# Optimization experiments

Hardware: AMD Instinct MI355X
Metric: run time of the kernel (lower is better)

## Reference

```python
import jax, jax.numpy as jnp
import numpy as np

B, L, D = 8, 4096, 1024   # batch, max words, sent_dim
S, SENT_LEN = 255, 16     # sentences per sample, words per sentence (255*16=4080)
START_BOUND = 1           # leading zero-pad region, as in the torch module


def setup_inputs() -> dict:
    key = jax.random.key(0)
    k1, k2, k3, k4 = jax.random.split(key, 4)
    words_emb = jax.random.normal(k1, (B, L, D), jnp.float32)
    sents_emb = jax.random.normal(k2, (B, S, D), jnp.float32)
    # nn.Linear(2D, D): weight [D, 2D], bias [D]
    W1_w = jax.random.normal(k3, (D, 2 * D), jnp.float32) / np.sqrt(2 * D)
    W1_b = jax.random.normal(k4, (D,), jnp.float32) * 0.01
    # sentence-index-per-word map; -1 marks the zero-padded regions
    sm = -np.ones((B, L), np.int32)
    idx = np.repeat(np.arange(S, dtype=np.int32), SENT_LEN)  # [S*SENT_LEN]
    sm[:, START_BOUND:START_BOUND + S * SENT_LEN] = idx
    sent_map = jnp.asarray(sm)
    return {"words_emb": words_emb, "sents_emb": sents_emb,
            "W1_w": W1_w, "W1_b": W1_b, "sent_map": sent_map}


def reference(words_emb, sents_emb, W1_w, W1_b, sent_map):
    # Expand sentence embeddings to word positions via gather; zero outside spans.
    valid = sent_map >= 0                                    # [B, L]
    safe_idx = jnp.clip(sent_map, 0)                         # [B, L]
    gathered = jnp.take_along_axis(sents_emb, safe_idx[..., None], axis=1)  # [B, L, D]
    sents_state_flat = jnp.where(valid[..., None], gathered, 0.0)
    # concat word + sentence features, then Linear + ReLU
    x = jnp.concatenate([words_emb, sents_state_flat], axis=-1)  # [B, L, 2D]
    return jax.nn.relu(jnp.einsum('ble,de->bld', x, W1_w) + W1_b)
```

## Files before the change

### kernel.cpp

```cpp
#include <hip/hip_runtime.h>
#include <stdint.h>

constexpr int kB = 8;
constexpr int kL = 4096;
constexpr int kD = 1024;
constexpr int kS = 255;
constexpr int kM = kB * kL;
constexpr int kK = 2 * kD;
constexpr int kN = kD;

typedef __bf16 bf16x8 __attribute__((ext_vector_type(8)));
typedef float  f32x4  __attribute__((ext_vector_type(4)));

constexpr size_t WS_WORDS = 0;
constexpr size_t WS_SENTS = WS_WORDS + (size_t)kM * kD * 2;
constexpr size_t WS_W     = WS_SENTS + (size_t)kB * kS * kD * 2;
constexpr size_t WS_ZP    = WS_W + (size_t)kN * kK * 2;
constexpr size_t WS_NEED  = WS_ZP + 3072;

__device__ __forceinline__ uint32_t pk_bf16x2(float a, float b) {
    uint32_t ua = __float_as_uint(a) + 0x8000u;
    uint32_t ub = __float_as_uint(b) + 0x8000u;
    return __builtin_amdgcn_perm(ub, ua, 0x07060302u);
}

__device__ __forceinline__ void async16(const void* g, void* l) {
    __builtin_amdgcn_global_load_lds(
        (const __attribute__((address_space(1))) uint32_t*)g,
        (__attribute__((address_space(3))) uint32_t*)l, 16, 0, 0);
}

#define WAITVM(n)  asm volatile("s_waitcnt vmcnt(" #n ")" ::: "memory")
#define WAITLGKM0  asm volatile("s_waitcnt lgkmcnt(0)" ::: "memory")

__device__ __forceinline__ void blockbar() {
    __builtin_amdgcn_sched_barrier(0);
    __builtin_amdgcn_s_barrier();
    __builtin_amdgcn_sched_barrier(0);
}

__global__ __launch_bounds__(256)
void cvt_prepass2(const float4* __restrict__ words, const float4* __restrict__ sents,
                  const float4* __restrict__ W,
                  uint4* __restrict__ wordsB, uint4* __restrict__ sentsB,
                  uint4* __restrict__ WB, uint32_t* __restrict__ zp)
{
    constexpr size_t NW8 = (size_t)kM * kD / 8;
    constexpr size_t NS8 = (size_t)kB * kS * kD / 8;
    constexpr size_t NB8 = (size_t)kN * kK / 8;
    constexpr size_t NT8 = NW8 + NS8 + NB8;
    if (blockIdx.x == 0) {
        for (int t = threadIdx.x; t < 768; t += 256) zp[t] = 0u;
    }
    const size_t stride = (size_t)gridDim.x * blockDim.x;
    for (size_t i = (size_t)blockIdx.x * blockDim.x + threadIdx.x; i < NT8; i += stride) {
        const float4* src; uint4* dst; size_t j;
        if (i < NW8)            { src = words; dst = wordsB; j = i; }
        else if (i < NW8 + NS8) { src = sents; dst = sentsB; j = i - NW8; }
        else                    { src = W;     dst = WB;     j = i - NW8 - NS8; }
        float4 a  = src[2 * j];
        float4 b2 = src[2 * j + 1];
        uint4 o;
        o.x = pk_bf16x2(a.x,  a.y);
        o.y = pk_bf16x2(a.z,  a.w);
        o.z = pk_bf16x2(b2.x, b2.y);
        o.w = pk_bf16x2(b2.z, b2.w);
        dst[j] = o;
    }
}

__global__ __launch_bounds__(512, 2)
void wsib_gemm_v7(const uint8_t* __restrict__ wordsB,
                  const uint8_t* __restrict__ sentsB,
                  const uint8_t* __restrict__ WB,
                  const float*   __restrict__ bias,
                  const int*     __restrict__ smap,
                  const uint8_t* __restrict__ zp,
                  float* __restrict__ out)
{
    __shared__ uint8_t lds[4][2][16384];

    const int tid  = threadIdx.x;
    const int w    = tid >> 6;
    const int lane = tid & 63;
    const int nT = blockIdx.x;
    const int mT = blockIdx.y;

    const int wm = (w >> 2) * 128;
    const int wn = (w & 3) * 64;
    const int fr = lane & 15, quad = lane >> 4;
    const int lo = lane * 16;
    const int slabA = (w >> 2) * 8;
    const int slabB = (w & 3) * 4;

    float bv[4];
    #pragma unroll
    for (int ni = 0; ni < 4; ++ni) bv[ni] = bias[nT * 256 + wn + ni * 16 + fr];

    const int colb = quad * 16;
    const int r0 = w * 16 + fr, r1 = r0 + 128;
    const int gA0 = mT * 256 + r0, gA1 = mT * 256 + r1;
    const int bIdx = gA0 >> 12;
    const uint8_t* aw0 = wordsB + (size_t)gA0 * 2048 + colb;
    const uint8_t* aw1 = wordsB + (size_t)gA1 * 2048 + colb;
    const int s0 = smap[gA0], s1 = smap[gA1];
    const uint8_t* as0 = (s0 >= 0) ? sentsB + (size_t)(bIdx * kS + s0) * 2048 + colb : zp + colb;
    const uint8_t* as1 = (s1 >= 0) ? sentsB + (size_t)(bIdx * kS + s1) * 2048 + colb : zp + colb;
    const uint8_t* pB0 = WB + (size_t)(nT * 256 + r0) * 4096 + colb;
    const uint8_t* pB1 = WB + (size_t)(nT * 256 + r1) * 4096 + colb;

    auto stage = [&](int buf, int t) {
        uint8_t* A  = (uint8_t*)lds[buf][0];
        uint8_t* Bb = (uint8_t*)lds[buf][1];
        const uint8_t* a0 = (t < 32) ? aw0 + t * 64 : as0 + (t - 32) * 64;
        const uint8_t* a1 = (t < 32) ? aw1 + t * 64 : as1 + (t - 32) * 64;
        async16(a0, A + w * 1024);
        async16(a1, A + 8192 + w * 1024);
        async16(pB0 + t * 64, Bb + w * 1024);
        async16(pB1 + t * 64, Bb + 8192 + w * 1024);
    };

    f32x4 acc[8][4];
    #pragma unroll
    for (int i = 0; i < 8; ++i)
        #pragma unroll
        for (int j = 0; j < 4; ++j) acc[i][j] = (f32x4){0.f, 0.f, 0.f, 0.f};

    stage(0, 0);
    stage(1, 1);
    stage(2, 2);
    WAITVM(8);
    blockbar();

    bf16x8 af[4], bfA[4], bfB[4];
    #pragma unroll
    for (int mi = 0; mi < 4; ++mi)
        af[mi] = *(const bf16x8*)((uint8_t*)lds[0][0] + (slabA + mi) * 1024 + lo);
    #pragma unroll
    for (int ni = 0; ni < 4; ++ni)
        bfA[ni] = *(const bf16x8*)((uint8_t*)lds[0][1] + (slabB + ni) * 1024 + lo);

    auto kstep = [&](int t, bf16x8 (&bfc)[4], bf16x8 (&bfn)[4]) {
        uint8_t* bufT = (uint8_t*)lds[t & 3][0];

        bf16x8 ag[4];
        #pragma unroll
        for (int mi = 0; mi < 4; ++mi)
            ag[mi] = *(const bf16x8*)(bufT + (slabA + 4 + mi) * 1024 + lo);
        __builtin_amdgcn_s_setprio(1);
        #pragma unroll
        for (int mi = 0; mi < 4; ++mi)
            #pragma unroll
            for (int ni = 0; ni < 4; ++ni)
                acc[mi][ni] = __builtin_amdgcn_mfma_f32_16x16x32_bf16(
                    af[mi], bfc[ni], acc[mi][ni], 0, 0, 0);
        __builtin_amdgcn_s_setprio(0);

        WAITLGKM0;
        if (t < 62) { WAITVM(4); } else { WAITVM(0); }
        blockbar();

        if (t + 3 < 64) stage((t + 3) & 3, t + 3);
        if (t + 1 < 64) {
            uint8_t* bufNA = (uint8_t*)lds[(t + 1) & 3][0];
            uint8_t* bufNB = (uint8_t*)lds[(t + 1) & 3][1];
            #pragma unroll
            for (int ni = 0; ni < 4; ++ni)
                bfn[ni] = *(const bf16x8*)(bufNB + (slabB + ni) * 1024 + lo);
            #pragma unroll
            for (int mi = 0; mi < 4; ++mi)
                af[mi] = *(const bf16x8*)(bufNA + (slabA + mi) * 1024 + lo);
        }
        __builtin_amdgcn_s_setprio(1);
        #pragma unroll
        for (int mi = 0; mi < 4; ++mi)
            #pragma unroll
            for (int ni = 0; ni < 4; ++ni)
                acc[mi + 4][ni] = __builtin_amdgcn_mfma_f32_16x16x32_bf16(
                    ag[mi], bfc[ni], acc[mi + 4][ni], 0, 0, 0);
        __builtin_amdgcn_s_setprio(0);
    };

    #pragma unroll 1
    for (int t2 = 0; t2 < 32; ++t2) {
        kstep(2 * t2,     bfA, bfB);
        kstep(2 * t2 + 1, bfB, bfA);
    }

    const int rowBase = mT * 256 + wm + quad * 4;
    const int colBase = nT * 256 + wn + fr;
    #pragma unroll
    for (int mi = 0; mi < 8; ++mi) {
        #pragma unroll
        for (int ni = 0; ni < 4; ++ni) {
            const int col = colBase + ni * 16;
            #pragma unroll
            for (int r = 0; r < 4; ++r) {
                const int row = rowBase + mi * 16 + r;
                out[(size_t)row * kN + col] = fmaxf(acc[mi][ni][r] + bv[ni], 0.f);
            }
        }
    }
}

#define TILE_M 128
#define TILE_N 128
#define TILE_K 32
#define LDS_STRIDE 20
__global__ __launch_bounds__(256)
void wsib_gemm_fb(const float* __restrict__ words, const float* __restrict__ sents,
                  const float* __restrict__ W, const float* __restrict__ bias,
                  const int* __restrict__ smap, float* __restrict__ out)
{
    __shared__ uint32_t Asm[TILE_M * LDS_STRIDE];
    __shared__ uint32_t Bsm[TILE_N * LDS_STRIDE];
    const int tid = threadIdx.x, nT = blockIdx.x, mT = blockIdx.y;
    const int sRow = tid >> 1, half = tid & 1;
    const int mRow = mT * TILE_M + sRow, bIdx = mRow >> 12;
    const float* wsrc = words + (size_t)mRow * kD + half * 16;
    const int sidx = smap[mRow];
    const float* ssrc = (sidx >= 0) ? sents + ((size_t)bIdx * kS + sidx) * kD + half * 16 : nullptr;
    const float* bsrc = W + (size_t)(nT * TILE_N + sRow) * kK + half * 16;
    uint32_t* adst = &Asm[sRow * LDS_STRIDE + half * 8];
    uint32_t* bdst = &Bsm[sRow * LDS_STRIDE + half * 8];
    const int lane = tid & 63, wv = tid >> 6;
    const int wm = (wv & 1) * 64, wn = (wv >> 1) * 64;
    const int fr = lane & 15, quad = lane >> 4;
    f32x4 acc[4][4];
    #pragma unroll
    for (int i = 0; i < 4; ++i)
        #pragma unroll
        for (int j = 0; j < 4; ++j) acc[i][j] = (f32x4){0.f, 0.f, 0.f, 0.f};
    float4 ra[4], rb[4];
    {
        const float4* pa = (const float4*)wsrc; const float4* pb = (const float4*)bsrc;
        #pragma unroll
        for (int i = 0; i < 4; ++i) { ra[i] = pa[i]; rb[i] = pb[i]; }
    }
    for (int k0 = 0; k0 < kK; k0 += TILE_K) {
        uint32_t pa[8], pb[8];
        #pragma unroll
        for (int i = 0; i < 4; ++i) {
            pa[2*i] = pk_bf16x2(ra[i].x, ra[i].y); pa[2*i+1] = pk_bf16x2(ra[i].z, ra[i].w);
            pb[2*i] = pk_bf16x2(rb[i].x, rb[i].y); pb[2*i+1] = pk_bf16x2(rb[i].z, rb[i].w);
        }
        __syncthreads();
        ((uint4*)adst)[0] = make_uint4(pa[0], pa[1], pa[2], pa[3]);
        ((uint4*)adst)[1] = make_uint4(pa[4], pa[5], pa[6], pa[7]);
        ((uint4*)bdst)[0] = make_uint4(pb[0], pb[1], pb[2], pb[3]);
        ((uint4*)bdst)[1] = make_uint4(pb[4], pb[5], pb[6], pb[7]);
        __syncthreads();
        const int k1 = k0 + TILE_K;
        if (k1 < kK) {
            const float* asrc = (k1 < kD) ? (wsrc + k1) : (ssrc ? (ssrc + (k1 - kD)) : nullptr);
            if (asrc) { const float4* p = (const float4*)asrc;
                #pragma unroll
                for (int i = 0; i < 4; ++i) ra[i] = p[i];
            } else {
                #pragma unroll
                for (int i = 0; i < 4; ++i) ra[i] = make_float4(0.f, 0.f, 0.f, 0.f);
            }
            const float4* p = (const float4*)(bsrc + k1);
            #pragma unroll
            for (int i = 0; i < 4; ++i) rb[i] = p[i];
        }
        bf16x8 af[4], bfv[4];
        #pragma unroll
        for (int mi = 0; mi < 4; ++mi)
            af[mi] = *(const bf16x8*)&Asm[(wm + mi * 16 + fr) * LDS_STRIDE + quad * 4];
        #pragma unroll
        for (int ni = 0; ni < 4; ++ni)
            bfv[ni] = *(const bf16x8*)&Bsm[(wn + ni * 16 + fr) * LDS_STRIDE + quad * 4];
        #pragma unroll
        for (int mi = 0; mi < 4; ++mi)
            #pragma unroll
            for (int ni = 0; ni < 4; ++ni)
                acc[mi][ni] = __builtin_amdgcn_mfma_f32_16x16x32_bf16(af[mi], bfv[ni], acc[mi][ni], 0, 0, 0);
    }
    const int rowBase = mT * TILE_M + wm, colBase = nT * TILE_N + wn;
    float bv[4];
    #pragma unroll
    for (int ni = 0; ni < 4; ++ni) bv[ni] = bias[colBase + ni * 16 + fr];
    #pragma unroll
    for (int mi = 0; mi < 4; ++mi)
        #pragma unroll
        for (int ni = 0; ni < 4; ++ni) {
            const int col = colBase + ni * 16 + fr;
            #pragma unroll
            for (int r = 0; r < 4; ++r) {
                const int row = rowBase + mi * 16 + quad * 4 + r;
                out[(size_t)row * kN + col] = fmaxf(acc[mi][ni][r] + bv[ni], 0.f);
            }
        }
}

extern "C" void kernel_launch(void* const* d_in, const int* in_sizes, int n_in,
                              void* d_out, int out_size, void* d_ws, size_t ws_size,
                              hipStream_t stream) {
    const float* words = (const float*)d_in[0];
    const float* sents = (const float*)d_in[1];
    const float* W     = (const float*)d_in[2];
    const float* bias  = (const float*)d_in[3];
    const int*   smap  = (const int*)d_in[4];
    float* out = (float*)d_out;

    if (ws_size >= WS_NEED) {
        uint8_t* ws = (uint8_t*)d_ws;
        uint4* wordsB = (uint4*)(ws + WS_WORDS);
        uint4* sentsB = (uint4*)(ws + WS_SENTS);
        uint4* WB     = (uint4*)(ws + WS_W);
        uint32_t* zp  = (uint32_t*)(ws + WS_ZP);
        cvt_prepass2<<<2048, 256, 0, stream>>>(
            (const float4*)words, (const float4*)sents, (const float4*)W,
            wordsB, sentsB, WB, zp);
        dim3 grid(kN / 256, kM / 256);
        wsib_gemm_v7<<<grid, 512, 0, stream>>>(
            (const uint8_t*)wordsB, (const uint8_t*)sentsB, (const uint8_t*)WB,
            bias, smap, (const uint8_t*)zp, out);
    } else {
        dim3 grid(kN / TILE_N, kM / TILE_M);
        wsib_gemm_fb<<<grid, 256, 0, stream>>>(words, sents, W, bias, smap, out);
    }
}
```

Measured before the change: 372.2 us.

## Remap GEMM tiles per XCD and split A/B staging around MFMA phases

```diff
diff --git a/kernel.cpp b/kernel.cpp
--- a/kernel.cpp
+++ b/kernel.cpp
@@ -70,7 +70,7 @@
 }
 
 __global__ __launch_bounds__(512, 2)
-void wsib_gemm_v7(const uint8_t* __restrict__ wordsB,
+void wsib_gemm_v8(const uint8_t* __restrict__ wordsB,
                   const uint8_t* __restrict__ sentsB,
                   const uint8_t* __restrict__ WB,
                   const float*   __restrict__ bias,
@@ -83,8 +83,11 @@
     const int tid  = threadIdx.x;
     const int w    = tid >> 6;
     const int lane = tid & 63;
-    const int nT = blockIdx.x;
-    const int mT = blockIdx.y;
+
+    const int lin = blockIdx.y * gridDim.x + blockIdx.x;
+    const int swz = (lin & 7) * 64 + (lin >> 3);
+    const int nT = swz & 3;
+    const int mT = swz >> 2;
 
     const int wm = (w >> 2) * 128;
     const int wn = (w & 3) * 64;
@@ -109,13 +112,15 @@
     const uint8_t* pB0 = WB + (size_t)(nT * 256 + r0) * 4096 + colb;
     const uint8_t* pB1 = WB + (size_t)(nT * 256 + r1) * 4096 + colb;
 
-    auto stage = [&](int buf, int t) {
-        uint8_t* A  = (uint8_t*)lds[buf][0];
-        uint8_t* Bb = (uint8_t*)lds[buf][1];
+    auto stageA = [&](int buf, int t) {
+        uint8_t* A = (uint8_t*)lds[buf][0];
         const uint8_t* a0 = (t < 32) ? aw0 + t * 64 : as0 + (t - 32) * 64;
         const uint8_t* a1 = (t < 32) ? aw1 + t * 64 : as1 + (t - 32) * 64;
         async16(a0, A + w * 1024);
         async16(a1, A + 8192 + w * 1024);
+    };
+    auto stageB = [&](int buf, int t) {
+        uint8_t* Bb = (uint8_t*)lds[buf][1];
         async16(pB0 + t * 64, Bb + w * 1024);
         async16(pB1 + t * 64, Bb + 8192 + w * 1024);
     };
@@ -126,9 +131,9 @@
         #pragma unroll
         for (int j = 0; j < 4; ++j) acc[i][j] = (f32x4){0.f, 0.f, 0.f, 0.f};
 
-    stage(0, 0);
-    stage(1, 1);
-    stage(2, 2);
+    stageA(0, 0); stageB(0, 0);
+    stageA(1, 1); stageB(1, 1);
+    stageA(2, 2); stageB(2, 2);
     WAITVM(8);
     blockbar();
 
@@ -142,11 +147,17 @@
 
     auto kstep = [&](int t, bf16x8 (&bfc)[4], bf16x8 (&bfn)[4]) {
         uint8_t* bufT = (uint8_t*)lds[t & 3][0];
+        const int tS = (t + 3 < 64) ? t + 3 : 63;
+        const int bufS = (t + 3) & 3;
 
         bf16x8 ag[4];
         #pragma unroll
         for (int mi = 0; mi < 4; ++mi)
             ag[mi] = *(const bf16x8*)(bufT + (slabA + 4 + mi) * 1024 + lo);
+        stageA(bufS, tS);
+        blockbar();
+        WAITLGKM0;
+        __builtin_amdgcn_sched_barrier(0);
         __builtin_amdgcn_s_setprio(1);
         #pragma unroll
         for (int mi = 0; mi < 4; ++mi)
@@ -155,12 +166,9 @@
                 acc[mi][ni] = __builtin_amdgcn_mfma_f32_16x16x32_bf16(
                     af[mi], bfc[ni], acc[mi][ni], 0, 0, 0);
         __builtin_amdgcn_s_setprio(0);
-
-        WAITLGKM0;
-        if (t < 62) { WAITVM(4); } else { WAITVM(0); }
+        WAITVM(6);
         blockbar();
 
-        if (t + 3 < 64) stage((t + 3) & 3, t + 3);
         if (t + 1 < 64) {
             uint8_t* bufNA = (uint8_t*)lds[(t + 1) & 3][0];
             uint8_t* bufNB = (uint8_t*)lds[(t + 1) & 3][1];
@@ -171,6 +179,10 @@
             for (int mi = 0; mi < 4; ++mi)
                 af[mi] = *(const bf16x8*)(bufNA + (slabA + mi) * 1024 + lo);
         }
+        stageB(bufS, tS);
+        blockbar();
+        WAITLGKM0;
+        __builtin_amdgcn_sched_barrier(0);
         __builtin_amdgcn_s_setprio(1);
         #pragma unroll
         for (int mi = 0; mi < 4; ++mi)
@@ -179,6 +191,7 @@
                 acc[mi + 4][ni] = __builtin_amdgcn_mfma_f32_16x16x32_bf16(
                     ag[mi], bfc[ni], acc[mi + 4][ni], 0, 0, 0);
         __builtin_amdgcn_s_setprio(0);
+        blockbar();
     };
 
     #pragma unroll 1
@@ -314,7 +327,7 @@
             (const float4*)words, (const float4*)sents, (const float4*)W,
             wordsB, sentsB, WB, zp);
         dim3 grid(kN / 256, kM / 256);
-        wsib_gemm_v7<<<grid, 512, 0, stream>>>(
+        wsib_gemm_v8<<<grid, 512, 0, stream>>>(
             (const uint8_t*)wordsB, (const uint8_t*)sentsB, (const uint8_t*)WB,
             bias, smap, (const uint8_t*)zp, out);
     } else {
```

Result: no change. 378.2 us (+1.6%).
